# Optimization experiments

Measured on AMD Instinct MI355X. Metric: run time of the kernel, lower is better.

## Reference

```python
import jax, jax.numpy as jnp
import numpy as np

B, L, D = 4, 2048, 1024
H, DH = 16, 64  # heads, head dim (D = H*DH)


def setup_inputs() -> dict:
    key = jax.random.key(0)
    k1, k2, k3 = jax.random.split(key, 3)
    scale = D ** -0.5
    xin = jax.random.normal(k1, (B, L, D), dtype=jnp.float32)
    W_qkv = jax.random.normal(k2, (D, 3 * D), dtype=jnp.float32) * scale
    W_o = jax.random.normal(k3, (D, D), dtype=jnp.float32) * scale
    return {"xin": xin, "W_qkv": W_qkv, "W_o": W_o}


def reference(xin, W_qkv, W_o):
    b, Lq, _ = xin.shape
    # QKV projection: (b, L, 3D). NOTE: original torch code reshapes the
    # (b, L, 3D) buffer directly to (b, 3, H, L, DH) — a non-standard axis
    # interleave — which we replicate faithfully.
    QKV = (xin @ W_qkv).reshape(b, 3, H, Lq, DH)
    Q, K, V = QKV[:, 0], QKV[:, 1], QKV[:, 2]  # each (b, H, L, DH)
    scores = jnp.einsum("bhqd,bhkd->bhqk", Q, K) * (DH ** -0.5)
    attn = jax.nn.softmax(scores, axis=-1)  # dropout_prob=0.0 -> identity
    out = jnp.einsum("bhqk,bhkd->bhqd", attn, V)
    out = out.transpose(0, 2, 1, 3).reshape(b, Lq, H * DH)
    return out @ W_o
```

## Files before the change

### kernel.cpp

```cpp
#include <hip/hip_runtime.h>
#include <stdint.h>

typedef short short8 __attribute__((ext_vector_type(8)));
typedef float f32x4 __attribute__((ext_vector_type(4)));

#define LOG2E 1.44269504088896f
#define AS1 __attribute__((address_space(1)))
#define AS3 __attribute__((address_space(3)))

__device__ __forceinline__ float fexp2(float x) {
#if __has_builtin(__builtin_amdgcn_exp2f)
    return __builtin_amdgcn_exp2f(x);
#else
    return exp2f(x);
#endif
}
__device__ __forceinline__ unsigned short f2bfbits(float f) {
    unsigned x = __builtin_bit_cast(unsigned, f);
    unsigned r = x + 0x7fffu + ((x >> 16) & 1u);
    return (unsigned short)(r >> 16);
}
__device__ __forceinline__ float bfbits2f(unsigned short b) {
    unsigned u = ((unsigned)b) << 16;
    return __builtin_bit_cast(float, u);
}
__device__ __forceinline__ void unpack8(uint4 u, float4& f0, float4& f1) {
    f0.x = bfbits2f((unsigned short)(u.x & 0xffffu)); f0.y = bfbits2f((unsigned short)(u.x >> 16));
    f0.z = bfbits2f((unsigned short)(u.y & 0xffffu)); f0.w = bfbits2f((unsigned short)(u.y >> 16));
    f1.x = bfbits2f((unsigned short)(u.z & 0xffffu)); f1.y = bfbits2f((unsigned short)(u.z >> 16));
    f1.z = bfbits2f((unsigned short)(u.w & 0xffffu)); f1.w = bfbits2f((unsigned short)(u.w >> 16));
}
__device__ __forceinline__ unsigned pack2(float a, float b) {
    return (unsigned)f2bfbits(a) | ((unsigned)f2bfbits(b) << 16);
}
__device__ __forceinline__ unsigned pack2t(float a, float b) {
    unsigned ba = __builtin_bit_cast(unsigned, a);
    unsigned bb = __builtin_bit_cast(unsigned, b);
    return (ba >> 16) | (bb & 0xffff0000u);
}
__device__ __forceinline__ void glds16(const void* gp, void* lp) {
    __builtin_amdgcn_global_load_lds((const AS1 unsigned*)(uintptr_t)gp,
                                     (AS3 unsigned*)(unsigned)(uintptr_t)lp, 16, 0, 0);
}

__global__ __launch_bounds__(256) void xbf_k(const float* __restrict__ x,
                                             unsigned short* __restrict__ y) {
    int i = (blockIdx.x * 256 + threadIdx.x) * 4;
    float4 v = *(const float4*)(x + i);
    uint2 u;
    u.x = pack2(v.x, v.y);
    u.y = pack2(v.z, v.w);
    *(uint2*)(y + i) = u;
}

__global__ __launch_bounds__(256) void t32cvt_k(const float* __restrict__ src,
                                                unsigned short* __restrict__ dst,
                                                int R, int C) {
    __shared__ float tile[32][36];
    int t = threadIdx.x;
    int bx = blockIdx.x, by = blockIdx.y;
    int r = t >> 3, c0 = (t & 7) * 4;
    *(float4*)&tile[r][c0] = *(const float4*)(src + (size_t)(by * 32 + r) * C + bx * 32 + c0);
    __syncthreads();
    uint2 u;
    u.x = pack2(tile[c0 + 0][r], tile[c0 + 1][r]);
    u.y = pack2(tile[c0 + 2][r], tile[c0 + 3][r]);
    *(uint2*)(dst + (size_t)(bx * 32 + r) * R + by * 32 + c0) = u;
}

template <bool CF32>
__global__ __launch_bounds__(256) void gemm_k(const unsigned short* __restrict__ A,
                                              const unsigned short* __restrict__ Bt,
                                              void* __restrict__ Cv,
                                              int M, int N, int K) {
    __shared__ unsigned short sA[128 * 32];
    __shared__ unsigned short sB[128 * 32];
    int t = threadIdx.x;
    int wid = t >> 6, lane = t & 63;
    int wm = (wid >> 1) * 64, wn = (wid & 1) * 64;
    int lm = lane & 15, lq = lane >> 4;
    size_t m0 = (size_t)blockIdx.y * 128, n0 = (size_t)blockIdx.x * 128;
    int srow = t >> 2, scol = (t & 3) * 8;
    const unsigned short* ga0 = A + (m0 + srow) * K + scol;
    const unsigned short* ga1 = A + (m0 + 64 + srow) * K + scol;
    const unsigned short* gb0 = Bt + (n0 + srow) * K + scol;
    const unsigned short* gb1 = Bt + (n0 + 64 + srow) * K + scol;
    unsigned short* laA0 = &sA[wid * 512];
    unsigned short* laA1 = &sA[2048 + wid * 512];
    unsigned short* laB0 = &sB[wid * 512];
    unsigned short* laB1 = &sB[2048 + wid * 512];
    f32x4 acc[4][4] = {};
    for (int k0 = 0; k0 < K; k0 += 32) {
        __syncthreads();
        glds16(ga0 + k0, laA0);
        glds16(ga1 + k0, laA1);
        glds16(gb0 + k0, laB0);
        glds16(gb1 + k0, laB1);
        __syncthreads();
        short8 af[4], bfr[4];
        #pragma unroll
        for (int i = 0; i < 4; ++i) af[i] = *(const short8*)&sA[(wm + i * 16 + lm) * 32 + lq * 8];
        #pragma unroll
        for (int j = 0; j < 4; ++j) bfr[j] = *(const short8*)&sB[(wn + j * 16 + lm) * 32 + lq * 8];
        #pragma unroll
        for (int i = 0; i < 4; ++i)
            #pragma unroll
            for (int j = 0; j < 4; ++j)
                acc[i][j] = __builtin_amdgcn_mfma_f32_16x16x32_bf16(af[i], bfr[j], acc[i][j], 0, 0, 0);
    }
    #pragma unroll
    for (int i = 0; i < 4; ++i)
        #pragma unroll
        for (int j = 0; j < 4; ++j)
            #pragma unroll
            for (int r = 0; r < 4; ++r) {
                size_t row = m0 + wm + i * 16 + lq * 4 + r;
                size_t col = n0 + wn + j * 16 + lm;
                if (CF32) ((float*)Cv)[row * N + col] = acc[i][j][r];
                else ((unsigned short*)Cv)[row * N + col] = f2bfbits(acc[i][j][r]);
            }
}

__global__ __launch_bounds__(256) void vt_k(const unsigned short* __restrict__ qkv,
                                            unsigned short* __restrict__ vt) {
    __shared__ unsigned short tile[64 * 72];
    int kt = blockIdx.x, bh = blockIdx.y;
    int b = bh >> 4, h = bh & 15;
    const unsigned short* Vp = qkv + (size_t)b * 6291456 + 4194304 + (size_t)h * 131072;
    int t = threadIdx.x;
    int row = t >> 2, cc = (t & 3) * 16;
    const unsigned short* src = Vp + (size_t)(kt * 64 + row) * 64 + cc;
    *(uint4*)&tile[row * 72 + cc] = *(const uint4*)src;
    *(uint4*)&tile[row * 72 + cc + 8] = *(const uint4*)(src + 8);
    __syncthreads();
    unsigned v[8];
    #pragma unroll
    for (int j = 0; j < 8; ++j) {
        unsigned short a = tile[(cc + 2 * j) * 72 + row];
        unsigned short bsh = tile[(cc + 2 * j + 1) * 72 + row];
        v[j] = (unsigned)a | ((unsigned)bsh << 16);
    }
    unsigned short* dst = vt + ((size_t)bh * 64 + row) * 2048 + kt * 64 + cc;
    *(uint4*)dst = make_uint4(v[0], v[1], v[2], v[3]);
    *(uint4*)(dst + 8) = make_uint4(v[4], v[5], v[6], v[7]);
}

__global__ __launch_bounds__(256, 4) void attn_mfma(const unsigned short* __restrict__ qkv,
                                                    const unsigned short* __restrict__ vt,
                                                    unsigned short* __restrict__ aout) {
    __shared__ unsigned short Ks[64 * 72];
    __shared__ unsigned short Vs[64 * 72];
    __shared__ unsigned short Ps[4 * 32 * 72];
    int bid = blockIdx.x;
    int qt = bid & 15, h = (bid >> 4) & 15, b = bid >> 8;
    int t = threadIdx.x;
    int wave = t >> 6, lane = t & 63, lm = lane & 15, quad = lane >> 4;
    const unsigned short* Qb = qkv + (size_t)b * 6291456 + (size_t)h * 131072;
    const unsigned short* Kb = Qb + 2097152;
    const unsigned short* Vtb = vt + (size_t)(b * 16 + h) * 131072;
    int q0 = qt * 128 + wave * 32;

    const float qs = 0.125f * LOG2E;
    short8 qf[2][2];
    #pragma unroll
    for (int i = 0; i < 2; ++i)
        #pragma unroll
        for (int c = 0; c < 2; ++c) {
            uint4 u = *(const uint4*)(Qb + (size_t)(q0 + i * 16 + lm) * 64 + c * 32 + quad * 8);
            float4 f0, f1; unpack8(u, f0, f1);
            uint4 v;
            v.x = pack2(f0.x * qs, f0.y * qs);
            v.y = pack2(f0.z * qs, f0.w * qs);
            v.z = pack2(f1.x * qs, f1.y * qs);
            v.w = pack2(f1.z * qs, f1.w * qs);
            qf[i][c] = *(short8*)&v;
        }

    short8 ones;
    #pragma unroll
    for (int z = 0; z < 8; ++z) ones[z] = (short)0x3F80;

    f32x4 o[2][4] = {};
    f32x4 l_acc[2] = {};

    int srow = t >> 2, scol = (t & 3) * 16;
    unsigned short* psw = Ps + wave * (32 * 72);

    uint4 k0r, k1r, v0r, v1r;
    {
        const unsigned short* kp = Kb + (size_t)srow * 64 + scol;
        k0r = *(const uint4*)kp;
        k1r = *(const uint4*)(kp + 8);
        const unsigned short* vp = Vtb + (size_t)srow * 2048 + scol;
        v0r = *(const uint4*)vp;
        v1r = *(const uint4*)(vp + 8);
    }

    #pragma unroll 1
    for (int kt = 0; kt < 32; ++kt) {
        __syncthreads();
        *(uint4*)&Ks[srow * 72 + scol] = k0r;
        *(uint4*)&Ks[srow * 72 + scol + 8] = k1r;
        *(uint4*)&Vs[srow * 72 + scol] = v0r;
        *(uint4*)&Vs[srow * 72 + scol + 8] = v1r;
        __syncthreads();

        if (kt < 31) {
            const unsigned short* kp = Kb + (size_t)((kt + 1) * 64 + srow) * 64 + scol;
            k0r = *(const uint4*)kp;
            k1r = *(const uint4*)(kp + 8);
            const unsigned short* vp = Vtb + (size_t)srow * 2048 + (kt + 1) * 64 + scol;
            v0r = *(const uint4*)vp;
            v1r = *(const uint4*)(vp + 8);
        }

        #pragma unroll
        for (int j = 0; j < 4; ++j) {
            short8 kf0 = *(const short8*)&Ks[(j * 16 + lm) * 72 + quad * 8];
            short8 kf1 = *(const short8*)&Ks[(j * 16 + lm) * 72 + 32 + quad * 8];
            #pragma unroll
            for (int i = 0; i < 2; ++i) {
                f32x4 sf = {0.f, 0.f, 0.f, 0.f};
                sf = __builtin_amdgcn_mfma_f32_16x16x32_bf16(kf0, qf[i][0], sf, 0, 0, 0);
                sf = __builtin_amdgcn_mfma_f32_16x16x32_bf16(kf1, qf[i][1], sf, 0, 0, 0);
                uint2 u;
                u.x = pack2t(fexp2(sf[0]), fexp2(sf[1]));
                u.y = pack2t(fexp2(sf[2]), fexp2(sf[3]));
                *(uint2*)&psw[(i * 16 + lm) * 72 + j * 16 + quad * 4] = u;
            }
        }

        #pragma unroll
        for (int c = 0; c < 2; ++c) {
            short8 pf[2];
            #pragma unroll
            for (int i = 0; i < 2; ++i)
                pf[i] = *(const short8*)&psw[(i * 16 + lm) * 72 + c * 32 + quad * 8];
            #pragma unroll
            for (int jd = 0; jd < 4; ++jd) {
                short8 vf = *(const short8*)&Vs[(jd * 16 + lm) * 72 + c * 32 + quad * 8];
                #pragma unroll
                for (int i = 0; i < 2; ++i)
                    o[i][jd] = __builtin_amdgcn_mfma_f32_16x16x32_bf16(pf[i], vf, o[i][jd], 0, 0, 0);
            }
            #pragma unroll
            for (int i = 0; i < 2; ++i)
                l_acc[i] = __builtin_amdgcn_mfma_f32_16x16x32_bf16(pf[i], ones, l_acc[i], 0, 0, 0);
        }
    }
    #pragma unroll
    for (int i = 0; i < 2; ++i)
        #pragma unroll
        for (int r = 0; r < 4; ++r) {
            float inv = 1.f / l_acc[i][r];
            int q = q0 + i * 16 + quad * 4 + r;
            size_t rowbase = ((size_t)b * 2048 + q) * 1024 + h * 64;
            #pragma unroll
            for (int jd = 0; jd < 4; ++jd)
                aout[rowbase + jd * 16 + lm] = f2bfbits(o[i][jd][r] * inv);
        }
}

extern "C" void kernel_launch(void* const* d_in, const int* in_sizes, int n_in,
                              void* d_out, int out_size, void* d_ws, size_t ws_size,
                              hipStream_t stream) {
    const float* xin  = (const float*)d_in[0];
    const float* wqkv = (const float*)d_in[1];
    const float* wo   = (const float*)d_in[2];
    float* out = (float*)d_out;

    char* ws = (char*)d_ws;
    unsigned short* qkv   = (unsigned short*)(ws);
    unsigned short* attn  = (unsigned short*)(ws + 50331648);
    unsigned short* wqkvT = (unsigned short*)(ws + 67108864);
    unsigned short* woT   = (unsigned short*)(ws + 73400320);
    unsigned short* vt    = (unsigned short*)(ws + 75497472);
    unsigned short* xb    = (unsigned short*)(ws + 92274688);

    dim3 blk(256);
    xbf_k<<<dim3(8192), blk, 0, stream>>>(xin, xb);
    t32cvt_k<<<dim3(3072 / 32, 1024 / 32), blk, 0, stream>>>(wqkv, wqkvT, 1024, 3072);
    t32cvt_k<<<dim3(1024 / 32, 1024 / 32), blk, 0, stream>>>(wo, woT, 1024, 1024);
    gemm_k<false><<<dim3(3072 / 128, 8192 / 128), blk, 0, stream>>>(xb, wqkvT, qkv, 8192, 3072, 1024);
    vt_k<<<dim3(32, 64), blk, 0, stream>>>(qkv, vt);
    attn_mfma<<<dim3(1024), blk, 0, stream>>>(qkv, vt, attn);
    gemm_k<true><<<dim3(1024 / 128, 8192 / 128), blk, 0, stream>>>(attn, woT, out, 8192, 1024, 1024);
}
```

Baseline: 300.2 us.

## Keep softmax probabilities in registers and feed PV via 16x16x16 MFMA

The exponentiated score tile produced by the QK^T MFMA is now reused directly as the A operand of 16x16x16 bf16 MFMAs for the PV product and the row-sum, instead of going through a per-wave LDS P buffer. This removes the LDS store, the read-back and the P shared allocation, which also cuts LDS usage per block. In exchange the PV step issues twice as many smaller MFMAs (K=16 instead of 32), with narrower V fragment loads from LDS.

```diff
diff --git a/kernel.cpp b/kernel.cpp
--- a/kernel.cpp
+++ b/kernel.cpp
@@ -2,6 +2,7 @@
 #include <stdint.h>
 
 typedef short short8 __attribute__((ext_vector_type(8)));
+typedef short short4v __attribute__((ext_vector_type(4)));
 typedef float f32x4 __attribute__((ext_vector_type(4)));
 
 #define LOG2E 1.44269504088896f
@@ -37,6 +38,14 @@
     unsigned ba = __builtin_bit_cast(unsigned, a);
     unsigned bb = __builtin_bit_cast(unsigned, b);
     return (ba >> 16) | (bb & 0xffff0000u);
+}
+__device__ __forceinline__ f32x4 mfma16(short4v a, short4v b, f32x4 c) {
+#if __has_builtin(__builtin_amdgcn_mfma_f32_16x16x16bf16_1k)
+    return __builtin_amdgcn_mfma_f32_16x16x16bf16_1k(a, b, c, 0, 0, 0);
+#else
+    asm("v_mfma_f32_16x16x16_bf16 %0, %1, %2, %0" : "+v"(c) : "v"(a), "v"(b));
+    return c;
+#endif
 }
 __device__ __forceinline__ void glds16(const void* gp, void* lp) {
     __builtin_amdgcn_global_load_lds((const AS1 unsigned*)(uintptr_t)gp,
@@ -150,7 +159,6 @@
                                                     unsigned short* __restrict__ aout) {
     __shared__ unsigned short Ks[64 * 72];
     __shared__ unsigned short Vs[64 * 72];
-    __shared__ unsigned short Ps[4 * 32 * 72];
     int bid = blockIdx.x;
     int qt = bid & 15, h = (bid >> 4) & 15, b = bid >> 8;
     int t = threadIdx.x;
@@ -176,15 +184,14 @@
             qf[i][c] = *(short8*)&v;
         }
 
-    short8 ones;
-    #pragma unroll
-    for (int z = 0; z < 8; ++z) ones[z] = (short)0x3F80;
+    short4v ones4;
+    #pragma unroll
+    for (int z = 0; z < 4; ++z) ones4[z] = (short)0x3F80;
 
     f32x4 o[2][4] = {};
     f32x4 l_acc[2] = {};
 
     int srow = t >> 2, scol = (t & 3) * 16;
-    unsigned short* psw = Ps + wave * (32 * 72);
 
     uint4 k0r, k1r, v0r, v1r;
     {
@@ -214,6 +221,7 @@
             v1r = *(const uint4*)(vp + 8);
         }
 
+        short4v pf[2][4];
         #pragma unroll
         for (int j = 0; j < 4; ++j) {
             short8 kf0 = *(const short8*)&Ks[(j * 16 + lm) * 72 + quad * 8];
@@ -226,26 +234,22 @@
                 uint2 u;
                 u.x = pack2t(fexp2(sf[0]), fexp2(sf[1]));
                 u.y = pack2t(fexp2(sf[2]), fexp2(sf[3]));
-                *(uint2*)&psw[(i * 16 + lm) * 72 + j * 16 + quad * 4] = u;
+                pf[i][j] = *(short4v*)&u;
             }
         }
 
         #pragma unroll
-        for (int c = 0; c < 2; ++c) {
-            short8 pf[2];
-            #pragma unroll
-            for (int i = 0; i < 2; ++i)
-                pf[i] = *(const short8*)&psw[(i * 16 + lm) * 72 + c * 32 + quad * 8];
-            #pragma unroll
-            for (int jd = 0; jd < 4; ++jd) {
-                short8 vf = *(const short8*)&Vs[(jd * 16 + lm) * 72 + c * 32 + quad * 8];
-                #pragma unroll
-                for (int i = 0; i < 2; ++i)
-                    o[i][jd] = __builtin_amdgcn_mfma_f32_16x16x32_bf16(pf[i], vf, o[i][jd], 0, 0, 0);
+        for (int jd = 0; jd < 4; ++jd)
+            #pragma unroll
+            for (int j = 0; j < 4; ++j) {
+                short4v vf = *(const short4v*)&Vs[(jd * 16 + lm) * 72 + j * 16 + quad * 4];
+                o[0][jd] = mfma16(pf[0][j], vf, o[0][jd]);
+                o[1][jd] = mfma16(pf[1][j], vf, o[1][jd]);
             }
-            #pragma unroll
-            for (int i = 0; i < 2; ++i)
-                l_acc[i] = __builtin_amdgcn_mfma_f32_16x16x32_bf16(pf[i], ones, l_acc[i], 0, 0, 0);
+        #pragma unroll
+        for (int j = 0; j < 4; ++j) {
+            l_acc[0] = mfma16(pf[0][j], ones4, l_acc[0]);
+            l_acc[1] = mfma16(pf[1][j], ones4, l_acc[1]);
         }
     }
     #pragma unroll
```

After: 292.1 us. 1.03x faster.
